# Optimization experiments

Measured on AMD Instinct MI355X. Metric: run time of the kernel, lower is better.

The kernel has to match this reference:

```python
import jax, jax.numpy as jnp
import numpy as np

ATTN_LEN = 128  # init_kwargs attn_len


def _lstm(x, Wih, Whh, bih, bhh):
    """PyTorch-style LSTM (gate order i,f,g,o), scanning over axis 0 of x.
    x: (S, N, H_in) -> (S, N, H). Matches nn.LSTM applied to the given layout."""
    H = Whh.shape[1]
    n = x.shape[1]
    xp = x @ Wih.T + bih + bhh  # precompute input projection, fold both biases

    def step(carry, xt):
        h, c = carry
        gates = xt + h @ Whh.T
        i, f, g, o = jnp.split(gates, 4, axis=-1)
        i = jax.nn.sigmoid(i)
        f = jax.nn.sigmoid(f)
        g = jnp.tanh(g)
        o = jax.nn.sigmoid(o)
        c = f * c + i * g
        h = o * jnp.tanh(c)
        return (h, c), h

    init = (jnp.zeros((n, H), x.dtype), jnp.zeros((n, H), x.dtype))
    _, hs = jax.lax.scan(step, init, xp)
    return hs


def setup_inputs() -> dict:
    key = jax.random.key(0)
    ks = jax.random.split(key, 16)
    F_in, H = 257, 256
    B, T = 8, 2048
    s = 1.0 / np.sqrt(H)

    def w(k, shape):
        return jax.random.uniform(k, shape, jnp.float32, -s, s)

    return {
        "x": jax.random.normal(ks[0], (B, T, F_in), jnp.float32),
        "feat_w": w(ks[1], (H, F_in)), "feat_b": w(ks[2], (H,)),
        "k_Wih": w(ks[3], (4 * H, H)), "k_Whh": w(ks[4], (4 * H, H)),
        "k_bih": w(ks[5], (4 * H,)), "k_bhh": w(ks[6], (4 * H,)),
        "q_Wih": w(ks[7], (4 * H, H)), "q_Whh": w(ks[8], (4 * H, H)),
        "q_bih": w(ks[9], (4 * H,)), "q_bhh": w(ks[10], (4 * H,)),
        "score_w": w(ks[11], (H, H)),
        "enhance_w": w(ks[12], (H, 2 * H)), "enhance_b": w(ks[13], (H,)),
        "mask_w": w(ks[14], (F_in, H)), "mask_b": w(ks[15], (F_in,)),
    }


def reference(x, feat_w, feat_b, k_Wih, k_Whh, k_bih, k_bhh,
              q_Wih, q_Whh, q_bih, q_bhh, score_w,
              enhance_w, enhance_b, mask_w, mask_b):
    input_x = x
    h = jnp.tanh(x @ feat_w.T + feat_b)          # (B,T,H); dropout_p=0 -> identity
    # Faithful to source: nn.LSTM without batch_first scans along dim0 of x.
    k = _lstm(h, k_Wih, k_Whh, k_bih, k_bhh)     # (B,T,H)
    q = _lstm(h, q_Wih, q_Whh, q_bih, q_bhh)     # stacked_encoder=False -> q_enc(x)

    # bmm(score(q), k^T): batched over dim0, attention over dims 1-2
    s = jnp.einsum('bth,bsh->bts', q @ score_w.T, k)
    e = jnp.exp(s - jnp.max(s, axis=-1, keepdims=True))
    T = s.shape[-1]
    band = jnp.tril(jnp.ones((T, T), x.dtype)) * jnp.triu(jnp.ones((T, T), x.dtype), -ATTN_LEN)
    w_ = e * band                                 # tril then triu(-attn_len)
    w_ = w_ / (jnp.sum(w_, axis=-1, keepdims=True) + 1e-10)
    c = jnp.einsum('bts,bsh->bth', w_, k)

    out = jnp.tanh(jnp.concatenate([c, q], axis=-1) @ enhance_w.T + enhance_b)
    m = jax.nn.sigmoid(out @ mask_w.T + mask_b)
    return input_x * m, w_
```

## Files before the change

### kernel.cpp

```cpp
#include <hip/hip_runtime.h>
#include <math.h>


#define Bq 8
#define Tq 2048
#define Fq 257
#define Hq 256
#define TH (Tq*Hq)
#define KW 192
#define PLD 40
#define KTLD 40
#define Mq (Bq*Tq)

typedef __bf16 bf16_t;
typedef __bf16 bf16x8 __attribute__((ext_vector_type(8)));
typedef float f32x4 __attribute__((ext_vector_type(4)));

__device__ __forceinline__ float sigf(float x) { return 1.0f / (1.0f + __expf(-x)); }
__device__ __forceinline__ float tanh_f(float x) { return 1.0f - 2.0f / (__expf(2.0f * x) + 1.0f); }

#define CV_X   (Mq*288)
#define CV_FW  (256*288)
#define CV_WK  (1024*512)
#define CV_WQ  (1024*512)
#define CV_SC  (256*256)
#define CV_EN  (256*512)
#define CV_MK  (384*256)
#define CV_O1  CV_X
#define CV_O2  (CV_O1+CV_FW)
#define CV_O3  (CV_O2+CV_WK)
#define CV_O4  (CV_O3+CV_WQ)
#define CV_O5  (CV_O4+CV_SC)
#define CV_O6  (CV_O5+CV_EN)
#define CV_TOT (CV_O6+CV_MK)
#define CVB    (CV_TOT/8/256)

__global__ __launch_bounds__(256) void cvt_all(
    const float* __restrict__ x, const float* __restrict__ feat_w,
    const float* __restrict__ kWih, const float* __restrict__ kWhh,
    const float* __restrict__ qWih, const float* __restrict__ qWhh,
    const float* __restrict__ scorew, const float* __restrict__ enhw,
    const float* __restrict__ maskw, bf16_t* __restrict__ dst,
    const float* __restrict__ kbih, const float* __restrict__ kbhh,
    const float* __restrict__ qbih, const float* __restrict__ qbhh,
    float* __restrict__ bias_all)
{
    if (blockIdx.x == CVB) {
        const int i0 = threadIdx.x * 8;
#pragma unroll
        for (int e = 0; e < 8; ++e) {
            const int i = i0 + e;
            bias_all[i] = (i < 1024) ? kbih[i] + kbhh[i]
                                     : qbih[i - 1024] + qbhh[i - 1024];
        }
        return;
    }
    const int base = (blockIdx.x * 256 + threadIdx.x) * 8;
    bf16_t v[8];
#pragma unroll
    for (int e = 0; e < 8; ++e) {
        const int i = base + e;
        float f;
        if (i < CV_O1)      { const int r = i / 288, c = i - r * 288;
                              f = (c < Fq) ? x[(size_t)r * Fq + c] : 0.0f; }
        else if (i < CV_O2) { const int i2 = i - CV_O1, r = i2 / 288, c = i2 - r * 288;
                              f = (c < Fq) ? feat_w[r * Fq + c] : 0.0f; }
        else if (i < CV_O3) { const int i2 = i - CV_O2, r = i2 >> 9, c = i2 & 511;
                              f = (c < 256) ? kWih[r * 256 + c] : kWhh[r * 256 + c - 256]; }
        else if (i < CV_O4) { const int i2 = i - CV_O3, r = i2 >> 9, c = i2 & 511;
                              f = (c < 256) ? qWih[r * 256 + c] : qWhh[r * 256 + c - 256]; }
        else if (i < CV_O5) { f = scorew[i - CV_O4]; }
        else if (i < CV_O6) { f = enhw[i - CV_O5]; }
        else                { const int i2 = i - CV_O6, r = i2 >> 8, c = i2 & 255;
                              f = (r < Fq) ? maskw[r * 256 + c] : 0.0f; }
        v[e] = (bf16_t)f;
    }
    *(bf16x8*)(dst + base) = *(bf16x8*)v;
}

__device__ __forceinline__ const bf16_t* seg_ptr(
    const bf16_t* __restrict__ A1, int lda1, int K1,
    const bf16_t* __restrict__ A2, int lda2, int row, int k, int col8)
{
    return (k < K1) ? A1 + (size_t)row * lda1 + k + col8
                    : A2 + (size_t)row * lda2 + (k - K1) + col8;
}

template<int ACT, bool MULX, bool BF16OUT, bool F32OUT>
__global__ __launch_bounds__(256) void gemm_mfma(
    const bf16_t* __restrict__ A1, int lda1, int K1,
    const bf16_t* __restrict__ A2, int lda2, int K2,
    const bf16_t* __restrict__ W,
    const float* __restrict__ bias,
    const float* __restrict__ xm, int ldx,
    float* __restrict__ out, bf16_t* __restrict__ outbf, int ldo, int Nlog)
{
    __shared__ __align__(16) bf16_t As[64 * 32];
    __shared__ __align__(16) bf16_t Ws[128 * 32];
    const int tid = threadIdx.x;
    const int lane = tid & 63;
    const int wave = tid >> 6;
    const int wr = wave >> 1, wc = wave & 1;
    const int fr = lane & 15;
    const int fo = (lane >> 4) * 8;
    const int srow = tid >> 2;
    const int scol = (tid & 3) * 8;
    const int m0 = blockIdx.y * 64, n0 = blockIdx.x * 128;

    const int K = K1 + K2;
    const int ldw = K;

    uint4 ar = *(const uint4*)seg_ptr(A1, lda1, K1, A2, lda2, m0 + srow, 0, scol);
    uint4 w0 = *(const uint4*)(W + (size_t)(n0 + srow)      * ldw + scol);
    uint4 w1 = *(const uint4*)(W + (size_t)(n0 + srow + 64) * ldw + scol);

    f32x4 acc[2][4] = {};
    for (int k0 = 0; k0 < K; k0 += 32) {
        __syncthreads();
        *(uint4*)&As[srow * 32 + scol]        = ar;
        *(uint4*)&Ws[srow * 32 + scol]        = w0;
        *(uint4*)&Ws[(srow + 64) * 32 + scol] = w1;
        if (k0 + 32 < K) {
            ar = *(const uint4*)seg_ptr(A1, lda1, K1, A2, lda2, m0 + srow, k0 + 32, scol);
            w0 = *(const uint4*)(W + (size_t)(n0 + srow)      * ldw + k0 + 32 + scol);
            w1 = *(const uint4*)(W + (size_t)(n0 + srow + 64) * ldw + k0 + 32 + scol);
        }
        __syncthreads();
        bf16x8 af[2], bfr[4];
#pragma unroll
        for (int i = 0; i < 2; ++i) af[i]  = *(const bf16x8*)&As[(wr * 32 + i * 16 + fr) * 32 + fo];
#pragma unroll
        for (int j = 0; j < 4; ++j) bfr[j] = *(const bf16x8*)&Ws[(wc * 64 + j * 16 + fr) * 32 + fo];
#pragma unroll
        for (int i = 0; i < 2; ++i)
#pragma unroll
            for (int j = 0; j < 4; ++j)
                acc[i][j] = __builtin_amdgcn_mfma_f32_16x16x32_bf16(af[i], bfr[j], acc[i][j], 0, 0, 0);
    }

    const int rbase = (lane >> 4) * 4;
#pragma unroll
    for (int i = 0; i < 2; ++i) {
#pragma unroll
        for (int j = 0; j < 4; ++j) {
            const int n = n0 + wc * 64 + j * 16 + fr;
            if (n >= Nlog) continue;
            const float bv = bias ? bias[n] : 0.0f;
            const int m = m0 + wr * 32 + i * 16 + rbase;
#pragma unroll
            for (int r = 0; r < 4; ++r) {
                float v = acc[i][j][r] + bv;
                if (ACT == 1) v = tanh_f(v);
                else if (ACT == 2) v = sigf(v);
                if (MULX) v *= xm[(size_t)(m + r) * ldx + n];
                if (F32OUT) out[(size_t)(m + r) * ldo + n] = v;
                if (BF16OUT) outbf[(size_t)(m + r) * ldo + n] = (bf16_t)v;
            }
        }
    }
}

template<bool FIRST>
__global__ __launch_bounds__(256) void lstm_step(
    const bf16_t* __restrict__ hfb,
    const bf16_t* __restrict__ hkp, const bf16_t* __restrict__ hqp,
    const bf16_t* __restrict__ Wall, const float* __restrict__ bias_all,
    float* __restrict__ cst,
    bf16_t* __restrict__ hk, bf16_t* __restrict__ hq)
{
    __shared__ __align__(16) bf16_t As[64 * 32];
    __shared__ __align__(16) bf16_t Ws[128 * 32];
    const int z = blockIdx.z;
    const bf16_t* hprev = z ? hqp : hkp;
    const bf16_t* Wz = Wall + (size_t)z * (1024 * 512);
    float* c     = cst + (size_t)z * TH;
    bf16_t* hout = z ? hq : hk;

    const int tid = threadIdx.x, lane = tid & 63, wave = tid >> 6;
    const int wr = wave >> 1, wc = wave & 1;
    const int fr = lane & 15, rg = lane >> 4, fo = rg * 8;
    const int m0 = blockIdx.y * 64;
    const int jb = blockIdx.x * 32;

    const int s0 = tid >> 2, acol = (tid & 3) * 8;
    const int s1 = s0 + 64;
    const int wn0 = ((s0 >> 5) * 256) + jb + (s0 & 31);
    const int wn1 = ((s1 >> 5) * 256) + jb + (s1 & 31);

    constexpr int NIT = FIRST ? 8 : 16;

    f32x4 acc[2][4] = {};

    uint4 ar  = *(const uint4*)(hfb + (size_t)(m0 + s0) * Hq + acol);
    uint4 w0r = *(const uint4*)(Wz + (size_t)wn0 * 512 + acol);
    uint4 w1r = *(const uint4*)(Wz + (size_t)wn1 * 512 + acol);
#pragma unroll
    for (int t = 0; t < NIT; ++t) {
        if (t) __syncthreads();
        *(uint4*)&As[s0 * 32 + acol] = ar;
        *(uint4*)&Ws[s0 * 32 + acol] = w0r;
        *(uint4*)&Ws[s1 * 32 + acol] = w1r;
        if (t + 1 < NIT) {
            const int tn = t + 1;
            ar  = (tn < 8)
                ? *(const uint4*)(hfb   + (size_t)(m0 + s0) * Hq + tn * 32 + acol)
                : *(const uint4*)(hprev + (size_t)(m0 + s0) * Hq + (tn - 8) * 32 + acol);
            w0r = *(const uint4*)(Wz + (size_t)wn0 * 512 + tn * 32 + acol);
            w1r = *(const uint4*)(Wz + (size_t)wn1 * 512 + tn * 32 + acol);
        }
        __syncthreads();
        bf16x8 af[2], bg[4];
#pragma unroll
        for (int i = 0; i < 2; ++i) af[i] = *(const bf16x8*)&As[(wr * 32 + i * 16 + fr) * 32 + fo];
#pragma unroll
        for (int g = 0; g < 4; ++g) bg[g] = *(const bf16x8*)&Ws[(g * 32 + wc * 16 + fr) * 32 + fo];
#pragma unroll
        for (int i = 0; i < 2; ++i)
#pragma unroll
            for (int g = 0; g < 4; ++g)
                acc[i][g] = __builtin_amdgcn_mfma_f32_16x16x32_bf16(af[i], bg[g], acc[i][g], 0, 0, 0);
    }

    const int j = jb + wc * 16 + fr;
    float bs[4];
#pragma unroll
    for (int g = 0; g < 4; ++g) bs[g] = bias_all[z * 1024 + g * 256 + j];
#pragma unroll
    for (int i = 0; i < 2; ++i)
#pragma unroll
        for (int r = 0; r < 4; ++r) {
            const int t = m0 + wr * 32 + i * 16 + rg * 4 + r;
            const size_t ix = (size_t)t * Hq + j;
            const float gi = acc[i][0][r] + bs[0];
            const float gf = acc[i][1][r] + bs[1];
            const float gg = acc[i][2][r] + bs[2];
            const float go = acc[i][3][r] + bs[3];
            const float cn = FIRST ? sigf(gi) * tanh_f(gg)
                                   : sigf(gf) * c[ix] + sigf(gi) * tanh_f(gg);
            c[ix] = cn;
            hout[ix] = (bf16_t)(sigf(go) * tanh_f(cn));
        }
}

__global__ __launch_bounds__(256) void band_fused(
    const bf16_t* __restrict__ qsbf, const bf16_t* __restrict__ kbf,
    float* __restrict__ out1, bf16_t* __restrict__ c_att)
{
    __shared__ __align__(16) bf16_t Ks[8 * KW * 32];
    __shared__ __align__(16) bf16_t P[6 * 64 * PLD];
    __shared__ __align__(16) bf16_t KT[256 * KTLD];

    const int b = blockIdx.y;
    const int t0 = blockIdx.x * 64;
    const int u0 = t0 - 128;
    const int tid = threadIdx.x, lane = tid & 63, w = tid >> 6;
    const int fr = lane & 15, rg = lane >> 4, fo = rg * 8;
    const size_t kbase = (size_t)b * Tq;

#pragma unroll
    for (int it = 0; it < 24; ++it) {
        const int idx = it * 256 + tid;
        const int n  = idx >> 5;
        const int c8 = (idx & 31) * 8;
        uint4 v = {0, 0, 0, 0};
        const int u = u0 + n;
        if (u >= 0) v = *(const uint4*)(kbf + (kbase + u) * (size_t)Hq + c8);
        *(uint4*)&Ks[((c8 >> 5) * KW + n) * 32 + (c8 & 31)] = v;
    }
    __syncthreads();

    f32x4 acc[12] = {};
    const bf16_t* qrow = qsbf + (kbase + t0 + 16 * w + fr) * (size_t)Hq;
#pragma unroll
    for (int ks = 0; ks < 8; ++ks) {
        const bf16x8 aq = *(const bf16x8*)(qrow + ks * 32 + fo);
#pragma unroll
        for (int jf = 0; jf < 12; ++jf) {
            const bf16x8 bk = *(const bf16x8*)&Ks[(ks * KW + jf * 16 + fr) * 32 + fo];
            acc[jf] = __builtin_amdgcn_mfma_f32_16x16x32_bf16(aq, bk, acc[jf], 0, 0, 0);
        }
    }

    const int jmin = (128 - t0) > 0 ? (128 - t0) : 0;
    float mx[4] = {-3e38f, -3e38f, -3e38f, -3e38f};
#pragma unroll
    for (int jf = 0; jf < 12; ++jf)
#pragma unroll
        for (int r = 0; r < 4; ++r) {
            const int i = 16 * w + rg * 4 + r;
            const int j = jf * 16 + fr;
            if (j >= i && j <= i + 128 && j >= jmin)
                mx[r] = fmaxf(mx[r], acc[jf][r]);
        }
#pragma unroll
    for (int d = 1; d < 16; d <<= 1)
#pragma unroll
        for (int r = 0; r < 4; ++r) mx[r] = fmaxf(mx[r], __shfl_xor(mx[r], d));

    float ex[12][4];
    float sm[4] = {0.0f, 0.0f, 0.0f, 0.0f};
#pragma unroll
    for (int jf = 0; jf < 12; ++jf)
#pragma unroll
        for (int r = 0; r < 4; ++r) {
            const int i = 16 * w + rg * 4 + r;
            const int j = jf * 16 + fr;
            const bool v = (j >= i && j <= i + 128 && j >= jmin);
            const float e = v ? __expf(acc[jf][r] - mx[r]) : 0.0f;
            ex[jf][r] = e;
            sm[r] += e;
        }
#pragma unroll
    for (int d = 1; d < 16; d <<= 1)
#pragma unroll
        for (int r = 0; r < 4; ++r) sm[r] += __shfl_xor(sm[r], d);
    float inv[4];
#pragma unroll
    for (int r = 0; r < 4; ++r) inv[r] = 1.0f / (sm[r] + 1e-10f);

#pragma unroll
    for (int jf = 0; jf < 12; ++jf)
#pragma unroll
        for (int r = 0; r < 4; ++r) {
            const int i = 16 * w + rg * 4 + r;
            const int j = jf * 16 + fr;
            const float wv = ex[jf][r] * inv[r];
            if (u0 + j >= 0)
                out1[(kbase + t0 + i) * (size_t)Tq + (u0 + j)] = wv;
            P[((j >> 5) * 64 + i) * PLD + (j & 31)] = (bf16_t)wv;
        }

    {
        const int c4l = (u0 > 0 ? u0 : 0) >> 2;
        const int c4r = (u0 + KW) >> 2;
        const float4 z4 = {0.0f, 0.0f, 0.0f, 0.0f};
        for (int rr = 0; rr < 16; ++rr) {
            float* rowp = out1 + (kbase + t0 + 16 * w + rr) * (size_t)Tq;
            for (int c4 = lane; c4 < c4l; c4 += 64)
                *(float4*)(rowp + 4 * c4) = z4;
            for (int c4 = c4r + lane; c4 < Tq / 4; c4 += 64)
                *(float4*)(rowp + 4 * c4) = z4;
        }
    }

    f32x4 cacc[16] = {};
    for (int jc = 0; jc < 6; ++jc) {
        __syncthreads();
#pragma unroll
        for (int it = 0; it < 4; ++it) {
            const int idx = it * 256 + tid;
            const int jl = idx >> 5;
            const int hc = (idx & 31) * 8;
            const bf16x8 kv = *(const bf16x8*)&Ks[((hc >> 5) * KW + jc * 32 + jl) * 32 + (hc & 31)];
#pragma unroll
            for (int e = 0; e < 8; ++e) KT[(hc + e) * KTLD + jl] = kv[e];
        }
        __syncthreads();
        const bf16x8 pa = *(const bf16x8*)&P[(jc * 64 + 16 * w + fr) * PLD + fo];
#pragma unroll
        for (int hf = 0; hf < 16; ++hf) {
            const bf16x8 bk = *(const bf16x8*)&KT[(hf * 16 + fr) * KTLD + fo];
            cacc[hf] = __builtin_amdgcn_mfma_f32_16x16x32_bf16(pa, bk, cacc[hf], 0, 0, 0);
        }
    }

#pragma unroll
    for (int hf = 0; hf < 16; ++hf)
#pragma unroll
        for (int r = 0; r < 4; ++r) {
            const int i = 16 * w + rg * 4 + r;
            c_att[(kbase + t0 + i) * (size_t)Hq + hf * 16 + fr] = (bf16_t)cacc[hf][r];
        }
}

extern "C" void kernel_launch(void* const* d_in, const int* in_sizes, int n_in,
                              void* d_out, int out_size, void* d_ws, size_t ws_size,
                              hipStream_t stream)
{
    (void)in_sizes; (void)n_in; (void)out_size; (void)ws_size;
    const float* x        = (const float*)d_in[0];
    const float* feat_w   = (const float*)d_in[1];
    const float* feat_b   = (const float*)d_in[2];
    const float* k_Wih    = (const float*)d_in[3];
    const float* k_Whh    = (const float*)d_in[4];
    const float* k_bih    = (const float*)d_in[5];
    const float* k_bhh    = (const float*)d_in[6];
    const float* q_Wih    = (const float*)d_in[7];
    const float* q_Whh    = (const float*)d_in[8];
    const float* q_bih    = (const float*)d_in[9];
    const float* q_bhh    = (const float*)d_in[10];
    const float* score_w  = (const float*)d_in[11];
    const float* enhance_w= (const float*)d_in[12];
    const float* enhance_b= (const float*)d_in[13];
    const float* mask_w   = (const float*)d_in[14];
    const float* mask_b   = (const float*)d_in[15];

    float* out0 = (float*)d_out;
    float* out1 = out0 + (size_t)Bq * Tq * Fq;

    float* cst      = (float*)d_ws;
    float* bias_all = cst + (size_t)2 * TH;
    bf16_t* cvd = (bf16_t*)(bias_all + 2048);
    bf16_t* xbf     = cvd;
    bf16_t* featw   = cvd + CV_O1;
    bf16_t* Wall    = cvd + CV_O2;
    bf16_t* scw     = cvd + CV_O4;
    bf16_t* enw     = cvd + CV_O5;
    bf16_t* mkw     = cvd + CV_O6;
    bf16_t* hfeatbf = cvd + CV_TOT;
    bf16_t* hkbf    = hfeatbf + (size_t)Mq * Hq;
    bf16_t* hqbf    = hkbf + (size_t)Bq * TH;
    bf16_t* cattb   = hqbf + (size_t)Bq * TH;

    cvt_all<<<CVB + 1, 256, 0, stream>>>(
        x, feat_w, k_Wih, k_Whh, q_Wih, q_Whh, score_w, enhance_w, mask_w, cvd,
        k_bih, k_bhh, q_bih, q_bhh, bias_all);

    gemm_mfma<1, false, true, false><<<dim3(2, Mq / 64), 256, 0, stream>>>(
        xbf, 288, 288, nullptr, 0, 0, featw, feat_b, nullptr, 0,
        nullptr, hfeatbf, Hq, 1 << 30);

    lstm_step<true><<<dim3(8, Tq / 64, 2), 256, 0, stream>>>(
        hfeatbf, nullptr, nullptr, Wall, bias_all, cst, hkbf, hqbf);
    for (int b = 1; b < Bq; ++b)
        lstm_step<false><<<dim3(8, Tq / 64, 2), 256, 0, stream>>>(
            hfeatbf + (size_t)b * TH,
            hkbf + (size_t)(b - 1) * TH, hqbf + (size_t)(b - 1) * TH,
            Wall, bias_all, cst,
            hkbf + (size_t)b * TH, hqbf + (size_t)b * TH);

    bf16_t* qsbf = xbf;
    gemm_mfma<0, false, true, false><<<dim3(2, Mq / 64), 256, 0, stream>>>(
        hqbf, Hq, Hq, nullptr, 0, 0, scw, nullptr, nullptr, 0,
        nullptr, qsbf, Hq, 1 << 30);

    band_fused<<<dim3(Tq / 64, Bq), 256, 0, stream>>>(qsbf, hkbf, out1, cattb);

    bf16_t* outh = hfeatbf;
    gemm_mfma<1, false, true, false><<<dim3(2, Mq / 64), 256, 0, stream>>>(
        cattb, Hq, Hq, hqbf, Hq, Hq, enw, enhance_b, nullptr, 0,
        nullptr, outh, Hq, 1 << 30);

    gemm_mfma<2, true, false, true><<<dim3(3, Mq / 64), 256, 0, stream>>>(
        outh, Hq, Hq, nullptr, 0, 0, mkw, mask_b, x, Fq,
        out0, nullptr, Fq, Fq);
}
```

Before: 209.9 us.

## Fuse enhance and mask GEMMs into one kernel; double K-chunk per LSTM step iteration

The enhance GEMM (tanh) and the mask GEMM (sigmoid times x) now run in one kernel. The 64x256 enhance output tile stays in shared memory and feeds the mask GEMM directly, so the intermediate no longer goes to global memory and one launch is dropped. The LSTM step kernel now stages two 32-wide K chunks per barrier pair, halving the sync count per launch at the cost of more shared memory and registers. The fused kernel uses many accumulators (16 f32x4 plus 16 more), which may reduce occupancy, and it reads the mask weights straight from global memory.

```diff
diff --git a/kernel.cpp b/kernel.cpp
--- a/kernel.cpp
+++ b/kernel.cpp
@@ -11,6 +11,7 @@
 #define PLD 40
 #define KTLD 40
 #define Mq (Bq*Tq)
+#define OLD 264
 
 typedef __bf16 bf16_t;
 typedef __bf16 bf16x8 __attribute__((ext_vector_type(8)));
@@ -168,8 +169,8 @@
     float* __restrict__ cst,
     bf16_t* __restrict__ hk, bf16_t* __restrict__ hq)
 {
-    __shared__ __align__(16) bf16_t As[64 * 32];
-    __shared__ __align__(16) bf16_t Ws[128 * 32];
+    __shared__ __align__(16) bf16_t As[2][64 * 32];
+    __shared__ __align__(16) bf16_t Ws[2][128 * 32];
     const int z = blockIdx.z;
     const bf16_t* hprev = z ? hqp : hkp;
     const bf16_t* Wz = Wall + (size_t)z * (1024 * 512);
@@ -187,38 +188,55 @@
     const int wn0 = ((s0 >> 5) * 256) + jb + (s0 & 31);
     const int wn1 = ((s1 >> 5) * 256) + jb + (s1 & 31);
 
-    constexpr int NIT = FIRST ? 8 : 16;
+    constexpr int NIT = FIRST ? 4 : 8;
+
+    auto aptr = [&](int cc) -> const bf16_t* {
+        return (FIRST || cc < 8)
+            ? hfb   + (size_t)(m0 + s0) * Hq + cc * 32 + acol
+            : hprev + (size_t)(m0 + s0) * Hq + (cc - 8) * 32 + acol;
+    };
+
+    uint4 arH[2], w0H[2], w1H[2];
+#pragma unroll
+    for (int h = 0; h < 2; ++h) {
+        arH[h] = *(const uint4*)aptr(h);
+        w0H[h] = *(const uint4*)(Wz + (size_t)wn0 * 512 + h * 32 + acol);
+        w1H[h] = *(const uint4*)(Wz + (size_t)wn1 * 512 + h * 32 + acol);
+    }
 
     f32x4 acc[2][4] = {};
-
-    uint4 ar  = *(const uint4*)(hfb + (size_t)(m0 + s0) * Hq + acol);
-    uint4 w0r = *(const uint4*)(Wz + (size_t)wn0 * 512 + acol);
-    uint4 w1r = *(const uint4*)(Wz + (size_t)wn1 * 512 + acol);
 #pragma unroll
     for (int t = 0; t < NIT; ++t) {
         if (t) __syncthreads();
-        *(uint4*)&As[s0 * 32 + acol] = ar;
-        *(uint4*)&Ws[s0 * 32 + acol] = w0r;
-        *(uint4*)&Ws[s1 * 32 + acol] = w1r;
+#pragma unroll
+        for (int h = 0; h < 2; ++h) {
+            *(uint4*)&As[h][s0 * 32 + acol] = arH[h];
+            *(uint4*)&Ws[h][s0 * 32 + acol] = w0H[h];
+            *(uint4*)&Ws[h][s1 * 32 + acol] = w1H[h];
+        }
         if (t + 1 < NIT) {
-            const int tn = t + 1;
-            ar  = (tn < 8)
-                ? *(const uint4*)(hfb   + (size_t)(m0 + s0) * Hq + tn * 32 + acol)
-                : *(const uint4*)(hprev + (size_t)(m0 + s0) * Hq + (tn - 8) * 32 + acol);
-            w0r = *(const uint4*)(Wz + (size_t)wn0 * 512 + tn * 32 + acol);
-            w1r = *(const uint4*)(Wz + (size_t)wn1 * 512 + tn * 32 + acol);
+#pragma unroll
+            for (int h = 0; h < 2; ++h) {
+                const int cc = 2 * (t + 1) + h;
+                arH[h] = *(const uint4*)aptr(cc);
+                w0H[h] = *(const uint4*)(Wz + (size_t)wn0 * 512 + cc * 32 + acol);
+                w1H[h] = *(const uint4*)(Wz + (size_t)wn1 * 512 + cc * 32 + acol);
+            }
         }
         __syncthreads();
-        bf16x8 af[2], bg[4];
-#pragma unroll
-        for (int i = 0; i < 2; ++i) af[i] = *(const bf16x8*)&As[(wr * 32 + i * 16 + fr) * 32 + fo];
-#pragma unroll
-        for (int g = 0; g < 4; ++g) bg[g] = *(const bf16x8*)&Ws[(g * 32 + wc * 16 + fr) * 32 + fo];
-#pragma unroll
-        for (int i = 0; i < 2; ++i)
-#pragma unroll
-            for (int g = 0; g < 4; ++g)
-                acc[i][g] = __builtin_amdgcn_mfma_f32_16x16x32_bf16(af[i], bg[g], acc[i][g], 0, 0, 0);
+#pragma unroll
+        for (int h = 0; h < 2; ++h) {
+            bf16x8 af[2], bg[4];
+#pragma unroll
+            for (int i = 0; i < 2; ++i) af[i] = *(const bf16x8*)&As[h][(wr * 32 + i * 16 + fr) * 32 + fo];
+#pragma unroll
+            for (int g = 0; g < 4; ++g) bg[g] = *(const bf16x8*)&Ws[h][(g * 32 + wc * 16 + fr) * 32 + fo];
+#pragma unroll
+            for (int i = 0; i < 2; ++i)
+#pragma unroll
+                for (int g = 0; g < 4; ++g)
+                    acc[i][g] = __builtin_amdgcn_mfma_f32_16x16x32_bf16(af[i], bg[g], acc[i][g], 0, 0, 0);
+        }
     }
 
     const int j = jb + wc * 16 + fr;
@@ -240,6 +258,98 @@
             c[ix] = cn;
             hout[ix] = (bf16_t)(sigf(go) * tanh_f(cn));
         }
+}
+
+__global__ __launch_bounds__(256) void enmask(
+    const bf16_t* __restrict__ cattb, const bf16_t* __restrict__ hqbf,
+    const bf16_t* __restrict__ enw, const float* __restrict__ enhance_b,
+    const bf16_t* __restrict__ mkw, const float* __restrict__ mask_b,
+    const float* __restrict__ x, float* __restrict__ out0)
+{
+    __shared__ __align__(16) bf16_t As[64 * 32];
+    __shared__ __align__(16) bf16_t Ws[256 * 32];
+    __shared__ __align__(16) bf16_t outhS[64 * OLD];
+
+    const int tid = threadIdx.x, lane = tid & 63, w = tid >> 6;
+    const int fr = lane & 15, rg = lane >> 4, fo = rg * 8;
+    const int m0 = blockIdx.x * 64;
+    const int s0 = tid >> 2, acol = (tid & 3) * 8;
+
+    auto aptr1 = [&](int cc) -> const bf16_t* {
+        return (cc < 8) ? cattb + (size_t)(m0 + s0) * Hq + cc * 32 + acol
+                        : hqbf  + (size_t)(m0 + s0) * Hq + (cc - 8) * 32 + acol;
+    };
+    uint4 ar, wreg[4];
+    ar = *(const uint4*)aptr1(0);
+#pragma unroll
+    for (int p = 0; p < 4; ++p)
+        wreg[p] = *(const uint4*)(enw + (size_t)(s0 + 64 * p) * 512 + acol);
+
+    f32x4 acc1[16] = {};
+    for (int t = 0; t < 16; ++t) {
+        if (t) __syncthreads();
+        *(uint4*)&As[s0 * 32 + acol] = ar;
+#pragma unroll
+        for (int p = 0; p < 4; ++p)
+            *(uint4*)&Ws[(s0 + 64 * p) * 32 + acol] = wreg[p];
+        if (t + 1 < 16) {
+            ar = *(const uint4*)aptr1(t + 1);
+#pragma unroll
+            for (int p = 0; p < 4; ++p)
+                wreg[p] = *(const uint4*)(enw + (size_t)(s0 + 64 * p) * 512 + (t + 1) * 32 + acol);
+        }
+        __syncthreads();
+        const bf16x8 af = *(const bf16x8*)&As[(w * 16 + fr) * 32 + fo];
+#pragma unroll
+        for (int hf = 0; hf < 16; ++hf) {
+            const bf16x8 bg = *(const bf16x8*)&Ws[(hf * 16 + fr) * 32 + fo];
+            acc1[hf] = __builtin_amdgcn_mfma_f32_16x16x32_bf16(af, bg, acc1[hf], 0, 0, 0);
+        }
+    }
+    __syncthreads();
+#pragma unroll
+    for (int hf = 0; hf < 16; ++hf) {
+        const int col = hf * 16 + fr;
+        const float bv = enhance_b[col];
+#pragma unroll
+        for (int r = 0; r < 4; ++r) {
+            const int row = w * 16 + rg * 4 + r;
+            outhS[row * OLD + col] = (bf16_t)tanh_f(acc1[hf][r] + bv);
+        }
+    }
+    __syncthreads();
+
+    for (int nt = w; nt < 6; nt += 4) {
+        f32x4 acc2[4][4] = {};
+#pragma unroll
+        for (int ks = 0; ks < 8; ++ks) {
+            bf16x8 af[4], bg[4];
+#pragma unroll
+            for (int it = 0; it < 4; ++it)
+                af[it] = *(const bf16x8*)&outhS[(it * 16 + fr) * OLD + ks * 32 + fo];
+#pragma unroll
+            for (int jt = 0; jt < 4; ++jt)
+                bg[jt] = *(const bf16x8*)(mkw + (size_t)(nt * 64 + jt * 16 + fr) * 256 + ks * 32 + fo);
+#pragma unroll
+            for (int it = 0; it < 4; ++it)
+#pragma unroll
+                for (int jt = 0; jt < 4; ++jt)
+                    acc2[it][jt] = __builtin_amdgcn_mfma_f32_16x16x32_bf16(af[it], bg[jt], acc2[it][jt], 0, 0, 0);
+        }
+#pragma unroll
+        for (int it = 0; it < 4; ++it)
+#pragma unroll
+            for (int jt = 0; jt < 4; ++jt) {
+                const int n = nt * 64 + jt * 16 + fr;
+                if (n >= Fq) continue;
+                const float mb = mask_b[n];
+#pragma unroll
+                for (int r = 0; r < 4; ++r) {
+                    const int m = m0 + it * 16 + rg * 4 + r;
+                    out0[(size_t)m * Fq + n] = x[(size_t)m * Fq + n] * sigf(acc2[it][jt][r] + mb);
+                }
+            }
+    }
 }
 
 __global__ __launch_bounds__(256) void band_fused(
@@ -436,12 +546,6 @@
 
     band_fused<<<dim3(Tq / 64, Bq), 256, 0, stream>>>(qsbf, hkbf, out1, cattb);
 
-    bf16_t* outh = hfeatbf;
-    gemm_mfma<1, false, true, false><<<dim3(2, Mq / 64), 256, 0, stream>>>(
-        cattb, Hq, Hq, hqbf, Hq, Hq, enw, enhance_b, nullptr, 0,
-        nullptr, outh, Hq, 1 << 30);
-
-    gemm_mfma<2, true, false, true><<<dim3(3, Mq / 64), 256, 0, stream>>>(
-        outh, Hq, Hq, nullptr, 0, 0, mkw, mask_b, x, Fq,
-        out0, nullptr, Fq, Fq);
-}
+    enmask<<<Mq / 64, 256, 0, stream>>>(
+        cattb, hqbf, enw, enhance_b, mkw, mask_b, x, out0);
+}
```

Result: slower. 350.7 us, median of 3 (+67.1%).

## Fuse score projection GEMM into band attention kernel; prefetch LSTM cell state

Applied to the files above, without the earlier changes.

Removes the separate q@score_w GEMM launch and computes the 64x256 projected query tile inside band_fused with MFMA, staging it in shared memory that aliases the P/KT buffers. This drops one kernel launch and the global round trip of the projected queries. The price is more shared-memory use and extra score_w reads from global in every block. Separately, the LSTM step loads the previous cell state and biases before the GEMM loop so their latency overlaps with the matrix work, at the cost of more live registers.

```diff
diff --git a/kernel.cpp b/kernel.cpp
--- a/kernel.cpp
+++ b/kernel.cpp
@@ -10,6 +10,7 @@
 #define KW 192
 #define PLD 40
 #define KTLD 40
+#define QLD 264
 #define Mq (Bq*Tq)
 
 typedef __bf16 bf16_t;
@@ -189,11 +190,24 @@
 
     constexpr int NIT = FIRST ? 8 : 16;
 
-    f32x4 acc[2][4] = {};
+    const int j = jb + wc * 16 + fr;
+    float bs[4];
+#pragma unroll
+    for (int g = 0; g < 4; ++g) bs[g] = bias_all[z * 1024 + g * 256 + j];
+    float cpre[2][4];
+    if (!FIRST) {
+#pragma unroll
+        for (int i = 0; i < 2; ++i)
+#pragma unroll
+            for (int r = 0; r < 4; ++r)
+                cpre[i][r] = c[(size_t)(m0 + wr * 32 + i * 16 + rg * 4 + r) * Hq + j];
+    }
 
     uint4 ar  = *(const uint4*)(hfb + (size_t)(m0 + s0) * Hq + acol);
     uint4 w0r = *(const uint4*)(Wz + (size_t)wn0 * 512 + acol);
     uint4 w1r = *(const uint4*)(Wz + (size_t)wn1 * 512 + acol);
+
+    f32x4 acc[2][4] = {};
 #pragma unroll
     for (int t = 0; t < NIT; ++t) {
         if (t) __syncthreads();
@@ -221,10 +235,6 @@
                 acc[i][g] = __builtin_amdgcn_mfma_f32_16x16x32_bf16(af[i], bg[g], acc[i][g], 0, 0, 0);
     }
 
-    const int j = jb + wc * 16 + fr;
-    float bs[4];
-#pragma unroll
-    for (int g = 0; g < 4; ++g) bs[g] = bias_all[z * 1024 + g * 256 + j];
 #pragma unroll
     for (int i = 0; i < 2; ++i)
 #pragma unroll
@@ -236,19 +246,22 @@
             const float gg = acc[i][2][r] + bs[2];
             const float go = acc[i][3][r] + bs[3];
             const float cn = FIRST ? sigf(gi) * tanh_f(gg)
-                                   : sigf(gf) * c[ix] + sigf(gi) * tanh_f(gg);
+                                   : sigf(gf) * cpre[i][r] + sigf(gi) * tanh_f(gg);
             c[ix] = cn;
             hout[ix] = (bf16_t)(sigf(go) * tanh_f(cn));
         }
 }
 
 __global__ __launch_bounds__(256) void band_fused(
-    const bf16_t* __restrict__ qsbf, const bf16_t* __restrict__ kbf,
+    const bf16_t* __restrict__ hqbf, const bf16_t* __restrict__ scw,
+    const bf16_t* __restrict__ kbf,
     float* __restrict__ out1, bf16_t* __restrict__ c_att)
 {
     __shared__ __align__(16) bf16_t Ks[8 * KW * 32];
-    __shared__ __align__(16) bf16_t P[6 * 64 * PLD];
-    __shared__ __align__(16) bf16_t KT[256 * KTLD];
+    __shared__ __align__(16) bf16_t Puni[6 * 64 * PLD + 256 * KTLD];
+    bf16_t* const P   = Puni;
+    bf16_t* const KT  = Puni + 6 * 64 * PLD;
+    bf16_t* const qsS = Puni;
 
     const int b = blockIdx.y;
     const int t0 = blockIdx.x * 64;
@@ -267,19 +280,38 @@
         if (u >= 0) v = *(const uint4*)(kbf + (kbase + u) * (size_t)Hq + c8);
         *(uint4*)&Ks[((c8 >> 5) * KW + n) * 32 + (c8 & 31)] = v;
     }
+
+    {
+        f32x4 sacc[16] = {};
+        const bf16_t* qrow = hqbf + (kbase + t0 + 16 * w + fr) * (size_t)Hq;
+#pragma unroll
+        for (int ks = 0; ks < 8; ++ks) {
+            const bf16x8 aq = *(const bf16x8*)(qrow + ks * 32 + fo);
+#pragma unroll
+            for (int nf = 0; nf < 16; ++nf) {
+                const bf16x8 bsw = *(const bf16x8*)(scw + (size_t)(nf * 16 + fr) * 256 + ks * 32 + fo);
+                sacc[nf] = __builtin_amdgcn_mfma_f32_16x16x32_bf16(aq, bsw, sacc[nf], 0, 0, 0);
+            }
+        }
+#pragma unroll
+        for (int nf = 0; nf < 16; ++nf)
+#pragma unroll
+            for (int r = 0; r < 4; ++r)
+                qsS[(16 * w + rg * 4 + r) * QLD + nf * 16 + fr] = (bf16_t)sacc[nf][r];
+    }
     __syncthreads();
 
     f32x4 acc[12] = {};
-    const bf16_t* qrow = qsbf + (kbase + t0 + 16 * w + fr) * (size_t)Hq;
 #pragma unroll
     for (int ks = 0; ks < 8; ++ks) {
-        const bf16x8 aq = *(const bf16x8*)(qrow + ks * 32 + fo);
+        const bf16x8 aq = *(const bf16x8*)&qsS[(16 * w + fr) * QLD + ks * 32 + fo];
 #pragma unroll
         for (int jf = 0; jf < 12; ++jf) {
             const bf16x8 bk = *(const bf16x8*)&Ks[(ks * KW + jf * 16 + fr) * 32 + fo];
             acc[jf] = __builtin_amdgcn_mfma_f32_16x16x32_bf16(aq, bk, acc[jf], 0, 0, 0);
         }
     }
+    __syncthreads();
 
     const int jmin = (128 - t0) > 0 ? (128 - t0) : 0;
     float mx[4] = {-3e38f, -3e38f, -3e38f, -3e38f};
@@ -429,12 +461,7 @@
             Wall, bias_all, cst,
             hkbf + (size_t)b * TH, hqbf + (size_t)b * TH);
 
-    bf16_t* qsbf = xbf;
-    gemm_mfma<0, false, true, false><<<dim3(2, Mq / 64), 256, 0, stream>>>(
-        hqbf, Hq, Hq, nullptr, 0, 0, scw, nullptr, nullptr, 0,
-        nullptr, qsbf, Hq, 1 << 30);
-
-    band_fused<<<dim3(Tq / 64, Bq), 256, 0, stream>>>(qsbf, hkbf, out1, cattb);
+    band_fused<<<dim3(Tq / 64, Bq), 256, 0, stream>>>(hqbf, scw, hkbf, out1, cattb);
 
     bf16_t* outh = hfeatbf;
     gemm_mfma<1, false, true, false><<<dim3(2, Mq / 64), 256, 0, stream>>>(
```

New measurement: 215.2 us. 1.02x slower.
